# Kernel optimization log

Measured on AMD Instinct MI355X. Metric: run time of the kernel, lower is better.

## Reference

```python
import jax, jax.numpy as jnp
import numpy as np
import math

H, C, PQ, PV = 12, 16, 4, 8  # heads, head dim, query points, value points
C_S, C_Z = 384, 128
W_C = math.sqrt(2.0 / (9.0 * PQ))
W_L = math.sqrt(1.0 / 3.0)


def setup_inputs() -> dict:
    key = jax.random.key(0)
    ks = jax.random.split(key, 14)
    B, N = 1, 768
    s = jax.random.normal(ks[0], (B, N, C_S), dtype=jnp.float32)
    z = jax.random.normal(ks[1], (B, N, N, C_Z), dtype=jnp.float32)
    R = jax.random.normal(ks[2], (B, N, 3, 3), dtype=jnp.float32)
    t = jax.random.normal(ks[3], (B, N, 3), dtype=jnp.float32)

    def lin(k, fan_in, fan_out):
        return jax.random.normal(k, (fan_in, fan_out), dtype=jnp.float32) / math.sqrt(fan_in)

    out_in = H * C + H * PV * 3 + H * C_Z  # 2016
    return {
        "single_representation": s,
        "pair_representation": z,
        "rotations": R,
        "translation": t,
        "W_q": lin(ks[4], C_S, H * C),
        "W_k": lin(ks[5], C_S, H * C),
        "W_v": lin(ks[6], C_S, H * C),
        "W_qp": lin(ks[7], C_S, 3 * H * PQ),
        "W_kp": lin(ks[8], C_S, 3 * H * PQ),
        "W_vp": lin(ks[9], C_S, 3 * H * PV),
        "W_b": lin(ks[10], C_Z, H),
        "W_out": lin(ks[11], out_in, C_S),
        "b_out": jnp.zeros((C_S,), dtype=jnp.float32),
    }


def reference(single_representation, pair_representation, rotations, translation,
              W_q, W_k, W_v, W_qp, W_kp, W_vp, W_b, W_out, b_out):
    s, z, R, t = single_representation, pair_representation, rotations, translation
    B, N, _ = s.shape

    # scalar q/k/v: [B,N,H,C]
    q = (s @ W_q).reshape(B, N, H, C)
    k = (s @ W_k).reshape(B, N, H, C)
    v = (s @ W_v).reshape(B, N, H, C)

    # local points -> global frames: x_glob = R x_loc + t
    def to_global(pts_flat, P):
        pts = pts_flat.reshape(B, N, H, P, 3)
        return jnp.einsum('bnij,bnhpj->bnhpi', R, pts) + t[:, :, None, None, :]

    q_pts = to_global(s @ W_qp, PQ)  # [B,N,H,PQ,3]
    k_pts = to_global(s @ W_kp, PQ)
    v_pts = to_global(s @ W_vp, PV)  # [B,N,H,PV,3]

    # scalar attention term
    qk = jnp.einsum('bnhc,bmhc->bhnm', q, k) / math.sqrt(C)
    # pair bias term
    bias = jnp.einsum('bnmz,zh->bhnm', z, W_b)
    # point distance term: sum_p ||q_i - k_j||^2 expanded to avoid [N,N,H,P,3]
    qn = jnp.sum(q_pts * q_pts, axis=(-2, -1))  # [B,N,H]
    kn = jnp.sum(k_pts * k_pts, axis=(-2, -1))
    cross = jnp.einsum('bnhpx,bmhpx->bhnm', q_pts, k_pts)
    sq_dist = qn.transpose(0, 2, 1)[:, :, :, None] + kn.transpose(0, 2, 1)[:, :, None, :] - 2.0 * cross

    logits = W_L * (qk + bias - 0.5 * W_C * sq_dist)  # [B,H,N,M]
    a = jax.nn.softmax(logits, axis=-1)

    # outputs
    o = jnp.einsum('bhnm,bmhc->bnhc', a, v).reshape(B, N, H * C)
    o_pts_g = jnp.einsum('bhnm,bmhpx->bnhpx', a, v_pts)
    # inverse frame: R^T (x - t)
    o_pts = jnp.einsum('bnij,bnhpi->bnhpj', R, o_pts_g - t[:, :, None, None, :])
    o_pts = o_pts.reshape(B, N, H * PV * 3)
    o_pair = jnp.einsum('bhnm,bnmz->bnhz', a, z).reshape(B, N, H * C_Z)

    cat = jnp.concatenate([o, o_pts, o_pair], axis=-1)  # [B,N,2016]
    return cat @ W_out + b_out  # [B,N,c_s]
```

## Files before the change

kernel.cpp:

```cpp
#include <hip/hip_runtime.h>
#include <math.h>

#define RAW_OFF    0u
#define VALL_OFF   884736u
#define KN_OFF     1081344u
#define CAT_OFF    1090560u
#define QP_OFF     1864704u
#define KP_OFF     2012160u
#define SLOG_OFF   2159616u
#define PART2_OFF  9237504u
#define WT_OFF     13089792u
#define SB_OFF     13476864u
#define WTC_OFF    13624320u

#define WL 0.5773502691896258f
#define WC 0.23570226039551587f
#define CKN (-0.5f*WL*WC)

typedef __attribute__((ext_vector_type(8))) short short8;
typedef __attribute__((ext_vector_type(4))) float f32x4;

__device__ __forceinline__ unsigned short f2bf1(float a) {
  unsigned u = __builtin_bit_cast(unsigned, a);
  return (unsigned short)((u + 0x7fff + ((u >> 16) & 1)) >> 16);
}
__device__ __forceinline__ unsigned f2bf2(float a, float b) {
  unsigned ua = __builtin_bit_cast(unsigned, a), ub = __builtin_bit_cast(unsigned, b);
  return (unsigned)((ua + 0x7fff + ((ua >> 16) & 1)) >> 16)
       | ((ub + 0x7fff + ((ub >> 16) & 1)) & 0xffff0000u);
}
__device__ __forceinline__ float bf2f(unsigned short u) {
  return __builtin_bit_cast(float, ((unsigned)u) << 16);
}
__device__ __forceinline__ float bflo(unsigned u) { return __builtin_bit_cast(float, u << 16); }
__device__ __forceinline__ float bfhi(unsigned u) { return __builtin_bit_cast(float, u & 0xffff0000u); }

#define BAR_LDS() asm volatile("s_waitcnt lgkmcnt(0)\n\ts_barrier" ::: "memory")

__global__ __launch_bounds__(256) void cvt_all(
    const float* __restrict__ s,
    const float* __restrict__ Wq, const float* __restrict__ Wk, const float* __restrict__ Wv,
    const float* __restrict__ Wqp, const float* __restrict__ Wkp, const float* __restrict__ Wvp,
    const float* __restrict__ Wout,
    unsigned short* __restrict__ sb, unsigned short* __restrict__ wtc,
    unsigned short* __restrict__ WT)
{
  __shared__ float tl[32][33];
  int b = blockIdx.x, t = threadIdx.x;
  if (b < 288) {
    int g = b*256 + t;
    float4 v = *(const float4*)(s + (size_t)g*4);
    uint2 p; p.x = f2bf2(v.x, v.y); p.y = f2bf2(v.z, v.w);
    *(uint2*)(sb + (size_t)g*4) = p;
  } else if (b < 720) {
    int g = (b-288)*256 + t;
    int c = g / 96, kq = (g % 96) * 4;
    const float* W; int od, cl;
    if (c < 192)      { W = Wq;  od = 192; cl = c; }
    else if (c < 384) { W = Wk;  od = 192; cl = c - 192; }
    else if (c < 576) { W = Wv;  od = 192; cl = c - 384; }
    else if (c < 720) { W = Wqp; od = 144; cl = c - 576; }
    else if (c < 864) { W = Wkp; od = 144; cl = c - 720; }
    else              { W = Wvp; od = 288; cl = c - 864; }
    float a = W[(size_t)(kq+0)*od + cl];
    float bb = W[(size_t)(kq+1)*od + cl];
    float d = W[(size_t)(kq+2)*od + cl];
    float e = W[(size_t)(kq+3)*od + cl];
    uint2 p; p.x = f2bf2(a, bb); p.y = f2bf2(d, e);
    *(uint2*)(wtc + (size_t)c*384 + kq) = p;
  } else {
    int bb = b - 720;
    int kt = bb % 63, ct = bb / 63;
    int k0 = kt*32, c0 = ct*32;
    int tr = t >> 5, tc = t & 31;
    #pragma unroll
    for (int i = 0; i < 4; ++i)
      tl[tr + i*8][tc] = Wout[(size_t)(k0 + tr + i*8)*384 + c0 + tc];
    __syncthreads();
    #pragma unroll
    for (int i = 0; i < 4; ++i) {
      int c = tr + i*8;
      WT[(size_t)(c0 + c)*2016 + k0 + tc] = f2bf1(tl[tc][c]);
    }
  }
}

__global__ __launch_bounds__(256) void prep_mfma(
    const unsigned short* __restrict__ sb, const unsigned short* __restrict__ wtc,
    float* __restrict__ raw)
{
  int t = threadIdx.x, b = blockIdx.x;
  int ct = b % 18, rt = b / 18;
  int lane = t & 63, wid = t >> 6;
  int l15 = lane & 15, kg = lane >> 4;
  int r0 = rt*64 + wid*16, c0 = ct*64;

  f32x4 acc[4];
  #pragma unroll
  for (int cs = 0; cs < 4; ++cs) acc[cs] = (f32x4){0.f,0.f,0.f,0.f};

  for (int k0 = 0; k0 < 384; k0 += 32) {
    short8 af = *(const short8*)(sb + (size_t)(r0 + l15)*384 + k0 + kg*8);
    #pragma unroll
    for (int cs = 0; cs < 4; ++cs) {
      short8 bf = *(const short8*)(wtc + (size_t)(c0 + cs*16 + l15)*384 + k0 + kg*8);
      acc[cs] = __builtin_amdgcn_mfma_f32_16x16x32_bf16(af, bf, acc[cs], 0, 0, 0);
    }
  }
  #pragma unroll
  for (int cs = 0; cs < 4; ++cs)
    #pragma unroll
    for (int r = 0; r < 4; ++r)
      raw[(size_t)(r0 + kg*4 + r)*1152 + c0 + cs*16 + l15] = acc[cs][r];
}

__global__ __launch_bounds__(256) void transform_qk(
    const float* __restrict__ raw, const float* __restrict__ R, const float* __restrict__ tg,
    float* __restrict__ kn, short* __restrict__ Qp, short* __restrict__ Kp,
    unsigned short* __restrict__ vall)
{
  int n = blockIdx.x, t = threadIdx.x;
  __shared__ float tl[576];
  const float* R9 = R + n*9;
  const float* tv = tg + n*3;
  #pragma unroll
  for (int i = 0; i < 3; ++i) {
    int j = i*256 + t;
    if (j >= 576) break;
    int jj, basecol;
    if (j < 144)      { jj = j;      basecol = 576; }
    else if (j < 288) { jj = j-144;  basecol = 720; }
    else              { jj = j-288;  basecol = 864; }
    int x = jj % 3;
    const float* p = raw + n*1152 + basecol + (jj - x);
    float val = R9[x*3+0]*p[0] + R9[x*3+1]*p[1] + R9[x*3+2]*p[2] + tv[x];
    tl[j] = val;
  }
  __syncthreads();
  if (t < 12) {
    const float* q = tl + 144 + t*12;
    float sm = 0.f;
    #pragma unroll
    for (int r = 0; r < 12; ++r) sm += q[r]*q[r];
    kn[n*12 + t] = sm;
  }
  for (int c = t; c < 480; c += 256) {
    float val = (c < 192) ? raw[n*1152 + 384 + c] : tl[288 + (c - 192)];
    vall[(size_t)n*512 + c] = f2bf1(val);
  }
  #pragma unroll
  for (int i = 0; i < 2; ++i) {
    int idx = i*256 + t;
    if (idx >= 384) break;
    int h = idx >> 5, k = idx & 31;
    float qv, kv;
    if (k < 16)      { qv = (WL*0.25f) * raw[n*1152 + h*16 + k];  kv = raw[n*1152 + 192 + h*16 + k]; }
    else if (k < 28) { qv = (WL*WC) * tl[h*12 + (k-16)];          kv = tl[144 + h*12 + (k-16)]; }
    else             { qv = 0.f; kv = 0.f; }
    Qp[n*384 + idx] = (short)f2bf1(qv);
    Kp[n*384 + idx] = (short)f2bf1(kv);
  }
}

__global__ __launch_bounds__(512) void logits_gemm(
    const short* __restrict__ Qp, const short* __restrict__ Kp,
    const float* __restrict__ kn, float* __restrict__ slog)
{
  int t = threadIdx.x, b = blockIdx.x;
  int bn = b / 12, bm = b % 12;
  int lane = t & 63, wid = t >> 6;
  int nsub = wid & 3, msub = wid >> 2;
  int l15 = lane & 15, kg = lane >> 4;
  int nrow = bn*64 + nsub*16 + l15;
  int mbase = bm*64 + msub*32;

  f32x4 acc[2][12];
  #pragma unroll
  for (int mt = 0; mt < 2; ++mt)
    #pragma unroll
    for (int h = 0; h < 12; ++h) acc[mt][h] = (f32x4){0.f,0.f,0.f,0.f};

  #pragma unroll
  for (int h = 0; h < 12; ++h) {
    short8 af = *(const short8*)(Qp + (size_t)(nrow*12 + h)*32 + kg*8);
    #pragma unroll
    for (int mt = 0; mt < 2; ++mt) {
      int m = mbase + mt*16 + l15;
      short8 bf = *(const short8*)(Kp + (size_t)(m*12 + h)*32 + kg*8);
      acc[mt][h] = __builtin_amdgcn_mfma_f32_16x16x32_bf16(af, bf, acc[mt][h], 0, 0, 0);
    }
  }
  #pragma unroll
  for (int mt = 0; mt < 2; ++mt) {
    int m = mbase + mt*16 + l15;
    float knadj[12];
    #pragma unroll
    for (int h = 0; h < 12; ++h) knadj[h] = CKN * kn[m*12 + h];
    #pragma unroll
    for (int r = 0; r < 4; ++r) {
      int nr = bn*64 + nsub*16 + kg*4 + r;
      size_t base = ((size_t)nr*768 + m)*12;
      #pragma unroll
      for (int hq = 0; hq < 3; ++hq) {
        float4 v;
        v.x = acc[mt][hq*4+0][r] + knadj[hq*4+0];
        v.y = acc[mt][hq*4+1][r] + knadj[hq*4+1];
        v.z = acc[mt][hq*4+2][r] + knadj[hq*4+2];
        v.w = acc[mt][hq*4+3][r] + knadj[hq*4+3];
        *(float4*)(slog + base + hq*4) = v;
      }
    }
  }
}

#define Z_L   0
#define BIASL 4352
#define PT    5440
#define S_L   6016
#define SMEMW 6028

__global__ __launch_bounds__(256, 2) void ipa_main(
    const float* __restrict__ z, const float* __restrict__ slog,
    const unsigned short* __restrict__ vall, const float* __restrict__ Wb,
    float* __restrict__ part2)
{
  __shared__ __align__(16) unsigned smem[SMEMW];
  float* smf = (float*)smem;
  unsigned short* lds16 = (unsigned short*)smem;
  int bx = blockIdx.x;
  int n = bx >> 1, hb = bx & 1;
  int t = threadIdx.x;
  int lane = t & 63, wid = t >> 6;
  int l15 = lane & 15, kg = lane >> 4;

  if (t < 12) smf[S_L + t] = 0.f;

  short8 wbf[4];
  {
    #pragma unroll
    for (int ks = 0; ks < 4; ++ks)
      #pragma unroll
      for (int e = 0; e < 8; ++e) {
        int kk = ks*32 + kg*8 + e;
        float v = (l15 < 12) ? WL * Wb[kk*12 + l15] : 0.f;
        wbf[ks][e] = (short)f2bf1(v);
      }
  }

  f32x4 oacc[2];
  oacc[0] = (f32x4){0.f,0.f,0.f,0.f};
  oacc[1] = (f32x4){0.f,0.f,0.f,0.f};

  bool dact = t < 240;
  int mh = t / 120, slot = t % 120;
  int dcol = (slot < 48) ? slot*4 : 192 + (slot-48)*4;
  int dh   = (slot < 48) ? (slot >> 2) : (slot-48)/6;
  const unsigned short* dsrc = vall + dcol;
  float da0 = 0.f, da1 = 0.f, da2 = 0.f, da3 = 0.f;

  const float* zrow = z + (size_t)n*768*128;
  int ssm = t >> 5, ssc = t & 31;

  float4 zst[8];
  #define STAGE_LOAD(M0)                                                     \
    _Pragma("unroll")                                                        \
    for (int i = 0; i < 8; ++i)                                              \
      zst[i] = *(const float4*)(zrow + (size_t)((M0) + i*8 + ssm)*128 + ssc*4);
  #define STAGE_WRITE()                                                      \
    _Pragma("unroll")                                                        \
    for (int i = 0; i < 8; ++i) {                                            \
      unsigned w0 = f2bf2(zst[i].x, zst[i].y);                               \
      unsigned w1 = f2bf2(zst[i].z, zst[i].w);                               \
      uint2 uu; uu.x = w0; uu.y = w1;                                        \
      *(uint2*)&smem[Z_L + (i*8 + ssm)*68 + ssc*2] = uu;                     \
    }

  const size_t slb = (size_t)n * 9216 + (size_t)hb * 4608;
  float4 sl, slnext;

  STAGE_LOAD(hb*384);
  if (t < 192) sl = *(const float4*)(slog + slb + t*4);
  STAGE_WRITE();
  BAR_LDS();

  for (int it = 0; it < 6; ++it) {
    int m0 = hb*384 + it*64;
    if (it < 5) {
      STAGE_LOAD(m0 + 64);
      if (t < 192) slnext = *(const float4*)(slog + slb + (size_t)(it+1)*768 + t*4);
    }

    {
      f32x4 bacc = (f32x4){0.f,0.f,0.f,0.f};
      int zbase = (wid*16 + l15)*68;
      #pragma unroll
      for (int ks = 0; ks < 4; ++ks) {
        short8 za = *(const short8*)&smem[Z_L + zbase + kg*4 + ks*16];
        bacc = __builtin_amdgcn_mfma_f32_16x16x32_bf16(za, wbf[ks], bacc, 0, 0, 0);
      }
      #pragma unroll
      for (int r = 0; r < 4; ++r)
        smf[BIASL + (wid*16 + kg*4 + r)*17 + l15] = bacc[r];
    }
    BAR_LDS();

    if (t < 192) {
      float slv[4] = {sl.x, sl.y, sl.z, sl.w};
      #pragma unroll
      for (int e = 0; e < 4; ++e) {
        int ge = t*4 + e;
        int m = ge / 12, h = ge - m*12;
        float p = __expf(slv[e] + smf[BIASL + m*17 + h]);
        lds16[PT*2 + h*72 + m] = f2bf1(p);
      }
    }
    BAR_LDS();

    if (t < 48) {
      int h = t >> 2, seg = t & 3;
      short8 a0 = *(const short8*)&lds16[PT*2 + h*72 + seg*16];
      short8 a1 = *(const short8*)&lds16[PT*2 + h*72 + seg*16 + 8];
      float ps = 0.f;
      #pragma unroll
      for (int e = 0; e < 8; ++e)
        ps += bf2f((unsigned short)a0[e]) + bf2f((unsigned short)a1[e]);
      ps += __shfl_xor(ps, 1);
      ps += __shfl_xor(ps, 2);
      if (seg == 0) smf[S_L + h] += ps;
    }

    {
      short8 af[2];
      #pragma unroll
      for (int ks = 0; ks < 2; ++ks)
        af[ks] = *(const short8*)&lds16[PT*2 + l15*72 + ks*32 + kg*8];
      #pragma unroll
      for (int tt = 0; tt < 2; ++tt) {
        int zc = (wid*2 + tt)*16 + l15;
        #pragma unroll
        for (int ks = 0; ks < 2; ++ks) {
          short8 bf;
          #pragma unroll
          for (int e = 0; e < 8; ++e)
            bf[e] = (short)lds16[Z_L*2 + (ks*32 + kg*8 + e)*136 + zc];
          oacc[tt] = __builtin_amdgcn_mfma_f32_16x16x32_bf16(af[ks], bf, oacc[tt], 0, 0, 0);
        }
      }
    }

    if (dact) {
      #pragma unroll
      for (int j4 = 0; j4 < 4; ++j4) {
        short8 pw = *(const short8*)&lds16[PT*2 + dh*72 + mh*32 + j4*8];
        #pragma unroll
        for (int e = 0; e < 8; ++e) {
          float wq = bf2f((unsigned short)pw[e]);
          int row = m0 + mh*32 + j4*8 + e;
          uint2 vv = *(const uint2*)(dsrc + (size_t)row*512);
          da0 += wq*bflo(vv.x); da1 += wq*bfhi(vv.x);
          da2 += wq*bflo(vv.y); da3 += wq*bfhi(vv.y);
        }
      }
    }

    if (it < 5) {
      BAR_LDS();
      STAGE_WRITE();
      if (t < 192) sl = slnext;
    }
    BAR_LDS();
  }

  float* pb = part2 + (size_t)bx * 2508;
  if (t < 12) pb[t] = smf[S_L + t];
  if (dact) {
    float4 dv; dv.x = da0; dv.y = da1; dv.z = da2; dv.w = da3;
    *(float4*)(pb + 12 + (mh*120 + slot)*4) = dv;
  }
  if (kg < 3) {
    #pragma unroll
    for (int tt = 0; tt < 2; ++tt) {
      int zc = (wid*2 + tt)*16 + l15;
      #pragma unroll
      for (int r = 0; r < 4; ++r)
        pb[972 + (kg*4 + r)*128 + zc] = oacc[tt][r];
    }
  }
}

__global__ __launch_bounds__(256) void combine(
    const float* __restrict__ part2, const float* __restrict__ Rg,
    const float* __restrict__ tg, unsigned short* __restrict__ catb)
{
  int n = blockIdx.x, t = threadIdx.x;
  const float* b0 = part2 + (size_t)n*2*2508;
  const float* b1 = b0 + 2508;
  __shared__ float S[12], ogl[288];
  if (t < 12) S[t] = b0[t] + b1[t];
  __syncthreads();
  unsigned short* cb = catb + (size_t)n*2016;
  for (int i = t; i < 480; i += 256) {
    float v = b0[12+i] + b0[12+480+i] + b1[12+i] + b1[12+480+i];
    int slot = i >> 2;
    int dh = (slot < 48) ? (slot >> 2) : ((slot - 48) / 6);
    float val = v / S[dh];
    if (i < 192) cb[i] = f2bf1(val);
    else         ogl[i - 192] = val;
  }
  __syncthreads();
  const float* R9 = Rg + n*9;
  const float* tv = tg + n*3;
  for (int j = t; j < 288; j += 256) {
    int x = j % 3, base = j - x;
    float g0 = ogl[base+0] - tv[0];
    float g1 = ogl[base+1] - tv[1];
    float g2 = ogl[base+2] - tv[2];
    cb[192 + j] = f2bf1(R9[x]*g0 + R9[3+x]*g1 + R9[6+x]*g2);
  }
  for (int e = t; e < 1536; e += 256) {
    int h = e >> 7;
    cb[480 + e] = f2bf1((b0[972+e] + b1[972+e]) / S[h]);
  }
}

__global__ __launch_bounds__(256) void final_mfma(
    const unsigned short* __restrict__ catb, const unsigned short* __restrict__ WT,
    const float* __restrict__ bout, float* __restrict__ out)
{
  int t = threadIdx.x, b = blockIdx.x;
  int rt = b / 6, ct = b % 6;
  int r0 = rt*64, c0 = ct*64;
  int lane = t & 63, wid = t >> 6;
  int l15 = lane & 15, kg = lane >> 4;

  f32x4 acc[4];
  #pragma unroll
  for (int cs = 0; cs < 4; ++cs) acc[cs] = (f32x4){0.f,0.f,0.f,0.f};

  const unsigned short* arow = catb + (size_t)(r0 + wid*16 + l15)*2016;
  for (int k0 = 0; k0 < 2016; k0 += 32) {
    short8 af = *(const short8*)(arow + k0 + kg*8);
    #pragma unroll
    for (int cs = 0; cs < 4; ++cs) {
      short8 bf = *(const short8*)(WT + (size_t)(c0 + cs*16 + l15)*2016 + k0 + kg*8);
      acc[cs] = __builtin_amdgcn_mfma_f32_16x16x32_bf16(af, bf, acc[cs], 0, 0, 0);
    }
  }
  #pragma unroll
  for (int cs = 0; cs < 4; ++cs) {
    #pragma unroll
    for (int r = 0; r < 4; ++r) {
      int nn = r0 + wid*16 + kg*4 + r;
      int c  = c0 + cs*16 + l15;
      out[(size_t)nn*384 + c] = acc[cs][r] + bout[c];
    }
  }
}

extern "C" void kernel_launch(void* const* d_in, const int* in_sizes, int n_in,
                              void* d_out, int out_size, void* d_ws, size_t ws_size,
                              hipStream_t stream) {
  const float* s    = (const float*)d_in[0];
  const float* z    = (const float*)d_in[1];
  const float* R    = (const float*)d_in[2];
  const float* tv   = (const float*)d_in[3];
  const float* Wq   = (const float*)d_in[4];
  const float* Wk   = (const float*)d_in[5];
  const float* Wv   = (const float*)d_in[6];
  const float* Wqp  = (const float*)d_in[7];
  const float* Wkp  = (const float*)d_in[8];
  const float* Wvp  = (const float*)d_in[9];
  const float* Wb   = (const float*)d_in[10];
  const float* Wout = (const float*)d_in[11];
  const float* bout = (const float*)d_in[12];
  float* out = (float*)d_out;
  float* ws  = (float*)d_ws;

  float* raw  = ws + RAW_OFF;
  unsigned short* vall = (unsigned short*)(ws + VALL_OFF);
  float* kn   = ws + KN_OFF;
  unsigned short* catb = (unsigned short*)(ws + CAT_OFF);
  short* Qp   = (short*)(ws + QP_OFF);
  short* Kp   = (short*)(ws + KP_OFF);
  float* slog = ws + SLOG_OFF;
  float* part2 = ws + PART2_OFF;
  unsigned short* WT = (unsigned short*)(ws + WT_OFF);
  unsigned short* sb = (unsigned short*)(ws + SB_OFF);
  unsigned short* wtc = (unsigned short*)(ws + WTC_OFF);

  cvt_all<<<1476, 256, 0, stream>>>(s, Wq, Wk, Wv, Wqp, Wkp, Wvp, Wout, sb, wtc, WT);
  prep_mfma<<<216, 256, 0, stream>>>(sb, wtc, raw);
  transform_qk<<<768, 256, 0, stream>>>(raw, R, tv, kn, Qp, Kp, vall);
  logits_gemm<<<144, 512, 0, stream>>>(Qp, Kp, kn, slog);
  ipa_main<<<1536, 256, 0, stream>>>(z, slog, vall, Wb, part2);
  combine<<<768, 256, 0, stream>>>(part2, R, tv, catb);
  final_mfma<<<72, 256, 0, stream>>>(catb, WT, bout, out);
}
```

Measured before the change: 183.7 us.

## Split fused IPA main kernel into probability, pair-output and value-output kernels

Replaces the single fused ipa_main (bias GEMM, exp, row sums, z-weighted and value-weighted accumulation per half row) plus the combine kernel with three kernels. pgen computes the pair bias and unnormalised probabilities per 64-column tile and writes them to a bf16 probability buffer with partial sums. opair streams z a second time with double-buffered LDS to form o_pair, and ovout does the value and point aggregation and normalisation. The logits are stored head-major so probabilities can be read contiguously. The intent is to remove the serialising barriers and low parallelism of the fused loop, at the cost of reading the large z tensor twice and an extra bf16 probability round trip through memory.

Result: slower. 273.7 us (+49.0%).

```diff
diff --git a/kernel.cpp b/kernel.cpp
--- a/kernel.cpp
+++ b/kernel.cpp
@@ -7,11 +7,12 @@
 #define CAT_OFF    1090560u
 #define QP_OFF     1864704u
 #define KP_OFF     2012160u
-#define SLOG_OFF   2159616u
-#define PART2_OFF  9237504u
-#define WT_OFF     13089792u
-#define SB_OFF     13476864u
-#define WTC_OFF    13624320u
+#define SLOG2_OFF  2159616u
+#define PB16_OFF   11596800u
+#define SPART_OFF  15139840u
+#define WT_OFF     15582208u
+#define SB_OFF     15969280u
+#define WTC_OFF    16116736u
 
 #define WL 0.5773502691896258f
 #define WC 0.23570226039551587f
@@ -164,7 +165,7 @@
 
 __global__ __launch_bounds__(512) void logits_gemm(
     const short* __restrict__ Qp, const short* __restrict__ Kp,
-    const float* __restrict__ kn, float* __restrict__ slog)
+    const float* __restrict__ kn, float* __restrict__ slog2)
 {
   int t = threadIdx.x, b = blockIdx.x;
   int bn = b / 12, bm = b % 12;
@@ -192,220 +193,204 @@
   }
   #pragma unroll
   for (int mt = 0; mt < 2; ++mt) {
-    int m = mbase + mt*16 + l15;
+    int mglob = mbase + mt*16 + l15;
+    int mlocal = msub*32 + mt*16 + l15;
     float knadj[12];
     #pragma unroll
-    for (int h = 0; h < 12; ++h) knadj[h] = CKN * kn[m*12 + h];
+    for (int h = 0; h < 12; ++h) knadj[h] = CKN * kn[mglob*12 + h];
     #pragma unroll
     for (int r = 0; r < 4; ++r) {
       int nr = bn*64 + nsub*16 + kg*4 + r;
-      size_t base = ((size_t)nr*768 + m)*12;
+      size_t base = ((size_t)nr*12 + bm)*1024 + mlocal;
       #pragma unroll
-      for (int hq = 0; hq < 3; ++hq) {
-        float4 v;
-        v.x = acc[mt][hq*4+0][r] + knadj[hq*4+0];
-        v.y = acc[mt][hq*4+1][r] + knadj[hq*4+1];
-        v.z = acc[mt][hq*4+2][r] + knadj[hq*4+2];
-        v.w = acc[mt][hq*4+3][r] + knadj[hq*4+3];
-        *(float4*)(slog + base + hq*4) = v;
-      }
-    }
-  }
-}
-
-#define Z_L   0
-#define BIASL 4352
-#define PT    5440
-#define S_L   6016
-#define SMEMW 6028
-
-__global__ __launch_bounds__(256, 2) void ipa_main(
-    const float* __restrict__ z, const float* __restrict__ slog,
-    const unsigned short* __restrict__ vall, const float* __restrict__ Wb,
-    float* __restrict__ part2)
-{
-  __shared__ __align__(16) unsigned smem[SMEMW];
-  float* smf = (float*)smem;
+      for (int h = 0; h < 12; ++h)
+        slog2[base + h*64] = acc[mt][h][r] + knadj[h];
+    }
+  }
+}
+
+__global__ __launch_bounds__(256) void pgen(
+    const float* __restrict__ z, const float* __restrict__ slog2,
+    const float* __restrict__ Wb, unsigned short* __restrict__ pb16,
+    float* __restrict__ Spart)
+{
+  int bx = blockIdx.x;
+  int n = bx / 12, mt = bx % 12, m0 = mt*64;
+  int t = threadIdx.x, lane = t & 63, wid = t >> 6;
+  int l15 = lane & 15, kg = lane >> 4;
+
+  short8 wbf[4];
+  #pragma unroll
+  for (int ks = 0; ks < 4; ++ks)
+    #pragma unroll
+    for (int e = 0; e < 8; ++e) {
+      int kk = ks*32 + kg*8 + e;
+      float v = (l15 < 12) ? WL * Wb[kk*12 + l15] : 0.f;
+      wbf[ks][e] = (short)f2bf1(v);
+    }
+
+  const float* zr = z + ((size_t)n*768 + m0 + wid*16 + l15)*128;
+  f32x4 bacc = (f32x4){0.f,0.f,0.f,0.f};
+  #pragma unroll
+  for (int ks = 0; ks < 4; ++ks) {
+    float4 a = *(const float4*)(zr + ks*32 + kg*8);
+    float4 b = *(const float4*)(zr + ks*32 + kg*8 + 4);
+    uint4 uu; uu.x = f2bf2(a.x, a.y); uu.y = f2bf2(a.z, a.w);
+    uu.z = f2bf2(b.x, b.y); uu.w = f2bf2(b.z, b.w);
+    short8 af = __builtin_bit_cast(short8, uu);
+    bacc = __builtin_amdgcn_mfma_f32_16x16x32_bf16(af, wbf[ks], bacc, 0, 0, 0);
+  }
+  float4 sl = *(const float4*)(slog2 + (size_t)n*12288 + mt*1024 + l15*64 + wid*16 + kg*4);
+  float pr0 = __expf(sl.x + bacc[0]);
+  float pr1 = __expf(sl.y + bacc[1]);
+  float pr2 = __expf(sl.z + bacc[2]);
+  float pr3 = __expf(sl.w + bacc[3]);
+  if (l15 < 12) {
+    uint2 pk; pk.x = f2bf2(pr0, pr1); pk.y = f2bf2(pr2, pr3);
+    *(uint2*)(pb16 + (size_t)n*9216 + l15*768 + m0 + wid*16 + kg*4) = pk;
+  }
+  float sacc = pr0 + pr1 + pr2 + pr3;
+  sacc += __shfl_xor(sacc, 16);
+  sacc += __shfl_xor(sacc, 32);
+  if (lane < 12) Spart[(size_t)(n*12 + lane)*48 + mt*4 + wid] = sacc;
+}
+
+#define OZ0 0
+#define OZ1 4352
+#define OSMEMW 8704
+
+__global__ __launch_bounds__(256, 2) void opair(
+    const float* __restrict__ z, const unsigned short* __restrict__ pb16,
+    const float* __restrict__ Spart, unsigned short* __restrict__ catb)
+{
+  __shared__ __align__(16) unsigned smem[OSMEMW];
   unsigned short* lds16 = (unsigned short*)smem;
-  int bx = blockIdx.x;
-  int n = bx >> 1, hb = bx & 1;
-  int t = threadIdx.x;
+  int n = blockIdx.x, t = threadIdx.x;
   int lane = t & 63, wid = t >> 6;
   int l15 = lane & 15, kg = lane >> 4;
-
-  if (t < 12) smf[S_L + t] = 0.f;
-
-  short8 wbf[4];
-  {
-    #pragma unroll
-    for (int ks = 0; ks < 4; ++ks)
-      #pragma unroll
-      for (int e = 0; e < 8; ++e) {
-        int kk = ks*32 + kg*8 + e;
-        float v = (l15 < 12) ? WL * Wb[kk*12 + l15] : 0.f;
-        wbf[ks][e] = (short)f2bf1(v);
-      }
-  }
 
   f32x4 oacc[2];
   oacc[0] = (f32x4){0.f,0.f,0.f,0.f};
   oacc[1] = (f32x4){0.f,0.f,0.f,0.f};
 
+  const float* zrow = z + (size_t)n*768*128;
+  int ssm = t >> 5, ssc = t & 31;
+
+  float4 zst[8];
+  #define OSTAGE_LOAD(M0)                                                    \
+    _Pragma("unroll")                                                        \
+    for (int i = 0; i < 8; ++i)                                              \
+      zst[i] = *(const float4*)(zrow + (size_t)((M0) + i*8 + ssm)*128 + ssc*4);
+  #define OSTAGE_WRITE(BASE)                                                 \
+    _Pragma("unroll")                                                        \
+    for (int i = 0; i < 8; ++i) {                                            \
+      unsigned w0 = f2bf2(zst[i].x, zst[i].y);                               \
+      unsigned w1 = f2bf2(zst[i].z, zst[i].w);                               \
+      uint2 uu; uu.x = w0; uu.y = w1;                                        \
+      *(uint2*)&smem[(BASE) + (i*8 + ssm)*68 + ssc*2] = uu;                  \
+    }
+
+  OSTAGE_LOAD(0);
+  OSTAGE_WRITE(OZ0);
+  BAR_LDS();
+
+  const unsigned short* prow = pb16 + (size_t)n*9216 + l15*768;
+
+  for (int it = 0; it < 12; ++it) {
+    int cur = (it & 1) ? OZ1 : OZ0;
+    int nxt = (it & 1) ? OZ0 : OZ1;
+    if (it < 11) OSTAGE_LOAD((it+1)*64);
+
+    short8 af[2];
+    #pragma unroll
+    for (int ks = 0; ks < 2; ++ks)
+      af[ks] = *(const short8*)(prow + it*64 + ks*32 + kg*8);
+    #pragma unroll
+    for (int tt = 0; tt < 2; ++tt) {
+      int zc = (wid*2 + tt)*16 + l15;
+      #pragma unroll
+      for (int ks = 0; ks < 2; ++ks) {
+        short8 bf;
+        #pragma unroll
+        for (int e = 0; e < 8; ++e)
+          bf[e] = (short)lds16[cur*2 + (ks*32 + kg*8 + e)*136 + zc];
+        oacc[tt] = __builtin_amdgcn_mfma_f32_16x16x32_bf16(af[ks], bf, oacc[tt], 0, 0, 0);
+      }
+    }
+    if (it < 11) OSTAGE_WRITE(nxt);
+    BAR_LDS();
+  }
+
+  if (kg < 3) {
+    unsigned short* cb = catb + (size_t)n*2016;
+    #pragma unroll
+    for (int r = 0; r < 4; ++r) {
+      int h = kg*4 + r;
+      float Ssum = 0.f;
+      const float* sp = Spart + (size_t)(n*12 + h)*48;
+      #pragma unroll
+      for (int q = 0; q < 48; ++q) Ssum += sp[q];
+      float inv = 1.f / Ssum;
+      #pragma unroll
+      for (int tt = 0; tt < 2; ++tt) {
+        int zc = (wid*2 + tt)*16 + l15;
+        cb[480 + h*128 + zc] = f2bf1(oacc[tt][r] * inv);
+      }
+    }
+  }
+}
+
+__global__ __launch_bounds__(256) void ovout(
+    const unsigned short* __restrict__ pb16, const unsigned short* __restrict__ vall,
+    const float* __restrict__ Spart, const float* __restrict__ Rg,
+    const float* __restrict__ tg, unsigned short* __restrict__ catb)
+{
+  int n = blockIdx.x, t = threadIdx.x;
+  __shared__ float ogl[288];
+  __shared__ float dred[480];
   bool dact = t < 240;
   int mh = t / 120, slot = t % 120;
   int dcol = (slot < 48) ? slot*4 : 192 + (slot-48)*4;
   int dh   = (slot < 48) ? (slot >> 2) : (slot-48)/6;
   const unsigned short* dsrc = vall + dcol;
+  const unsigned short* prow = pb16 + (size_t)n*9216 + dh*768;
   float da0 = 0.f, da1 = 0.f, da2 = 0.f, da3 = 0.f;
 
-  const float* zrow = z + (size_t)n*768*128;
-  int ssm = t >> 5, ssc = t & 31;
-
-  float4 zst[8];
-  #define STAGE_LOAD(M0)                                                     \
-    _Pragma("unroll")                                                        \
-    for (int i = 0; i < 8; ++i)                                              \
-      zst[i] = *(const float4*)(zrow + (size_t)((M0) + i*8 + ssm)*128 + ssc*4);
-  #define STAGE_WRITE()                                                      \
-    _Pragma("unroll")                                                        \
-    for (int i = 0; i < 8; ++i) {                                            \
-      unsigned w0 = f2bf2(zst[i].x, zst[i].y);                               \
-      unsigned w1 = f2bf2(zst[i].z, zst[i].w);                               \
-      uint2 uu; uu.x = w0; uu.y = w1;                                        \
-      *(uint2*)&smem[Z_L + (i*8 + ssm)*68 + ssc*2] = uu;                     \
-    }
-
-  const size_t slb = (size_t)n * 9216 + (size_t)hb * 4608;
-  float4 sl, slnext;
-
-  STAGE_LOAD(hb*384);
-  if (t < 192) sl = *(const float4*)(slog + slb + t*4);
-  STAGE_WRITE();
-  BAR_LDS();
-
-  for (int it = 0; it < 6; ++it) {
-    int m0 = hb*384 + it*64;
-    if (it < 5) {
-      STAGE_LOAD(m0 + 64);
-      if (t < 192) slnext = *(const float4*)(slog + slb + (size_t)(it+1)*768 + t*4);
-    }
-
-    {
-      f32x4 bacc = (f32x4){0.f,0.f,0.f,0.f};
-      int zbase = (wid*16 + l15)*68;
+  if (dact) {
+    for (int j8 = 0; j8 < 48; ++j8) {
+      int mb = mh*384 + j8*8;
+      short8 pw = *(const short8*)(prow + mb);
       #pragma unroll
-      for (int ks = 0; ks < 4; ++ks) {
-        short8 za = *(const short8*)&smem[Z_L + zbase + kg*4 + ks*16];
-        bacc = __builtin_amdgcn_mfma_f32_16x16x32_bf16(za, wbf[ks], bacc, 0, 0, 0);
+      for (int e = 0; e < 8; ++e) {
+        float wq = bf2f((unsigned short)pw[e]);
+        uint2 vv = *(const uint2*)(dsrc + (size_t)(mb + e)*512);
+        da0 += wq*bflo(vv.x); da1 += wq*bfhi(vv.x);
+        da2 += wq*bflo(vv.y); da3 += wq*bfhi(vv.y);
       }
-      #pragma unroll
-      for (int r = 0; r < 4; ++r)
-        smf[BIASL + (wid*16 + kg*4 + r)*17 + l15] = bacc[r];
-    }
-    BAR_LDS();
-
-    if (t < 192) {
-      float slv[4] = {sl.x, sl.y, sl.z, sl.w};
-      #pragma unroll
-      for (int e = 0; e < 4; ++e) {
-        int ge = t*4 + e;
-        int m = ge / 12, h = ge - m*12;
-        float p = __expf(slv[e] + smf[BIASL + m*17 + h]);
-        lds16[PT*2 + h*72 + m] = f2bf1(p);
-      }
-    }
-    BAR_LDS();
-
-    if (t < 48) {
-      int h = t >> 2, seg = t & 3;
-      short8 a0 = *(const short8*)&lds16[PT*2 + h*72 + seg*16];
-      short8 a1 = *(const short8*)&lds16[PT*2 + h*72 + seg*16 + 8];
-      float ps = 0.f;
-      #pragma unroll
-      for (int e = 0; e < 8; ++e)
-        ps += bf2f((unsigned short)a0[e]) + bf2f((unsigned short)a1[e]);
-      ps += __shfl_xor(ps, 1);
-      ps += __shfl_xor(ps, 2);
-      if (seg == 0) smf[S_L + h] += ps;
-    }
-
-    {
-      short8 af[2];
-      #pragma unroll
-      for (int ks = 0; ks < 2; ++ks)
-        af[ks] = *(const short8*)&lds16[PT*2 + l15*72 + ks*32 + kg*8];
-      #pragma unroll
-      for (int tt = 0; tt < 2; ++tt) {
-        int zc = (wid*2 + tt)*16 + l15;
-        #pragma unroll
-        for (int ks = 0; ks < 2; ++ks) {
-          short8 bf;
-          #pragma unroll
-          for (int e = 0; e < 8; ++e)
-            bf[e] = (short)lds16[Z_L*2 + (ks*32 + kg*8 + e)*136 + zc];
-          oacc[tt] = __builtin_amdgcn_mfma_f32_16x16x32_bf16(af[ks], bf, oacc[tt], 0, 0, 0);
-        }
-      }
-    }
-
-    if (dact) {
-      #pragma unroll
-      for (int j4 = 0; j4 < 4; ++j4) {
-        short8 pw = *(const short8*)&lds16[PT*2 + dh*72 + mh*32 + j4*8];
-        #pragma unroll
-        for (int e = 0; e < 8; ++e) {
-          float wq = bf2f((unsigned short)pw[e]);
-          int row = m0 + mh*32 + j4*8 + e;
-          uint2 vv = *(const uint2*)(dsrc + (size_t)row*512);
-          da0 += wq*bflo(vv.x); da1 += wq*bfhi(vv.x);
-          da2 += wq*bflo(vv.y); da3 += wq*bfhi(vv.y);
-        }
-      }
-    }
-
-    if (it < 5) {
-      BAR_LDS();
-      STAGE_WRITE();
-      if (t < 192) sl = slnext;
-    }
-    BAR_LDS();
-  }
-
-  float* pb = part2 + (size_t)bx * 2508;
-  if (t < 12) pb[t] = smf[S_L + t];
-  if (dact) {
+    }
+  }
+  if (dact && mh == 1) {
     float4 dv; dv.x = da0; dv.y = da1; dv.z = da2; dv.w = da3;
-    *(float4*)(pb + 12 + (mh*120 + slot)*4) = dv;
-  }
-  if (kg < 3) {
-    #pragma unroll
-    for (int tt = 0; tt < 2; ++tt) {
-      int zc = (wid*2 + tt)*16 + l15;
-      #pragma unroll
-      for (int r = 0; r < 4; ++r)
-        pb[972 + (kg*4 + r)*128 + zc] = oacc[tt][r];
-    }
-  }
-}
-
-__global__ __launch_bounds__(256) void combine(
-    const float* __restrict__ part2, const float* __restrict__ Rg,
-    const float* __restrict__ tg, unsigned short* __restrict__ catb)
-{
-  int n = blockIdx.x, t = threadIdx.x;
-  const float* b0 = part2 + (size_t)n*2*2508;
-  const float* b1 = b0 + 2508;
-  __shared__ float S[12], ogl[288];
-  if (t < 12) S[t] = b0[t] + b1[t];
+    *(float4*)&dred[slot*4] = dv;
+  }
   __syncthreads();
   unsigned short* cb = catb + (size_t)n*2016;
-  for (int i = t; i < 480; i += 256) {
-    float v = b0[12+i] + b0[12+480+i] + b1[12+i] + b1[12+480+i];
-    int slot = i >> 2;
-    int dh = (slot < 48) ? (slot >> 2) : ((slot - 48) / 6);
-    float val = v / S[dh];
-    if (i < 192) cb[i] = f2bf1(val);
-    else         ogl[i - 192] = val;
+  if (dact && mh == 0) {
+    float4 dr = *(const float4*)&dred[slot*4];
+    float Ssum = 0.f;
+    const float* sp = Spart + (size_t)(n*12 + dh)*48;
+    #pragma unroll
+    for (int q = 0; q < 48; ++q) Ssum += sp[q];
+    float inv = 1.f / Ssum;
+    float o0 = (da0+dr.x)*inv, o1 = (da1+dr.y)*inv;
+    float o2 = (da2+dr.z)*inv, o3 = (da3+dr.w)*inv;
+    if (slot < 48) {
+      cb[slot*4+0] = f2bf1(o0); cb[slot*4+1] = f2bf1(o1);
+      cb[slot*4+2] = f2bf1(o2); cb[slot*4+3] = f2bf1(o3);
+    } else {
+      int bse = (slot-48)*4;
+      ogl[bse+0] = o0; ogl[bse+1] = o1; ogl[bse+2] = o2; ogl[bse+3] = o3;
+    }
   }
   __syncthreads();
   const float* R9 = Rg + n*9;
@@ -416,10 +401,6 @@
     float g1 = ogl[base+1] - tv[1];
     float g2 = ogl[base+2] - tv[2];
     cb[192 + j] = f2bf1(R9[x]*g0 + R9[3+x]*g1 + R9[6+x]*g2);
-  }
-  for (int e = t; e < 1536; e += 256) {
-    int h = e >> 7;
-    cb[480 + e] = f2bf1((b0[972+e] + b1[972+e]) / S[h]);
   }
 }
 
@@ -482,8 +463,9 @@
   unsigned short* catb = (unsigned short*)(ws + CAT_OFF);
   short* Qp   = (short*)(ws + QP_OFF);
   short* Kp   = (short*)(ws + KP_OFF);
-  float* slog = ws + SLOG_OFF;
-  float* part2 = ws + PART2_OFF;
+  float* slog2 = ws + SLOG2_OFF;
+  unsigned short* pb16 = (unsigned short*)(ws + PB16_OFF);
+  float* Spart = ws + SPART_OFF;
   unsigned short* WT = (unsigned short*)(ws + WT_OFF);
   unsigned short* sb = (unsigned short*)(ws + SB_OFF);
   unsigned short* wtc = (unsigned short*)(ws + WTC_OFF);
@@ -491,8 +473,9 @@
   cvt_all<<<1476, 256, 0, stream>>>(s, Wq, Wk, Wv, Wqp, Wkp, Wvp, Wout, sb, wtc, WT);
   prep_mfma<<<216, 256, 0, stream>>>(sb, wtc, raw);
   transform_qk<<<768, 256, 0, stream>>>(raw, R, tv, kn, Qp, Kp, vall);
-  logits_gemm<<<144, 512, 0, stream>>>(Qp, Kp, kn, slog);
-  ipa_main<<<1536, 256, 0, stream>>>(z, slog, vall, Wb, part2);
-  combine<<<768, 256, 0, stream>>>(part2, R, tv, catb);
+  logits_gemm<<<144, 512, 0, stream>>>(Qp, Kp, kn, slog2);
+  pgen<<<9216, 256, 0, stream>>>(z, slog2, Wb, pb16, Spart);
+  opair<<<768, 256, 0, stream>>>(z, pb16, Spart, catb);
+  ovout<<<768, 256, 0, stream>>>(pb16, vall, Spart, R, tv, catb);
   final_mfma<<<72, 256, 0, stream>>>(catb, WT, bout, out);
 }
```
